# Kernel optimization log

Measured on AMD Instinct MI355X. Metric: run time of the kernel, lower is better.

The kernel has to match this reference:

```python
import jax, jax.numpy as jnp
import numpy as np

RANK = 64


def setup_inputs() -> dict:
    key = jax.random.key(0)
    ks = jax.random.split(key, 7)
    N, C, H, W, T = 32, 128, 32, 32, 12
    x = jax.random.normal(ks[0], (N, C, H, W, T), dtype=jnp.float32)
    ts_w = jax.random.normal(ks[1], (RANK, T, 3, 3), dtype=jnp.float32) * 0.1
    ts_b = jnp.zeros((RANK,), dtype=jnp.float32)
    tc_w = jax.random.normal(ks[2], (RANK, C), dtype=jnp.float32) * 0.1
    tc_b = jnp.zeros((RANK,), dtype=jnp.float32)
    sc_w = jax.random.normal(ks[3], (RANK, T), dtype=jnp.float32) * 0.1
    sc_b = jnp.zeros((RANK,), dtype=jnp.float32)
    return {"x": x, "ts_w": ts_w, "ts_b": ts_b, "tc_w": tc_w,
            "tc_b": tc_b, "sc_w": sc_w, "sc_b": sc_b}


def reference(x, ts_w, ts_b, tc_w, tc_b, sc_w, sc_b):
    # x: (N, C, H, W, T) -> internal layout (N, T, C, H, W)
    N, C, H, W, T = x.shape
    xt = jnp.transpose(x, (0, 4, 1, 2, 3))  # (N, T, C, H, W)

    # --- TS branch: channel-mean map -> conv(T -> rank, k3, pad1) -> sigmoid ---
    ts_in = jnp.mean(xt, axis=2)  # (N, T, H, W)
    ts = jax.lax.conv_general_dilated(
        ts_in, ts_w, window_strides=(1, 1), padding=[(1, 1), (1, 1)],
        dimension_numbers=("NCHW", "OIHW", "NCHW"))
    ts = ts + ts_b[None, :, None, None]
    TS = jax.nn.sigmoid(ts.reshape(N, RANK, H * W))  # (N, R, HW)

    # --- global spatial pooling: (N, T, C) ---
    pooled = jnp.mean(xt, axis=(3, 4))  # (N, T, C)

    # TC branch: Linear(C -> rank) then sigmoid -> (N, T, R)
    TC = jax.nn.sigmoid(pooled @ tc_w.T + tc_b)

    # SC branch: Linear(T -> rank) on (N, C, T) -> (N, C, R)
    SC = jax.nn.sigmoid(jnp.transpose(pooled, (0, 2, 1)) @ sc_w.T + sc_b)

    # rank-R CP reconstruction: result[n,t,c,s] = sum_r TS[n,r,s]*TC[n,t,r]*SC[n,c,r]
    result = jnp.einsum("nrs,ntr,ncr->ntcs", TS, TC, SC).reshape(N, T, C, H, W)

    res = jax.nn.relu(result * xt)  # (N, T, C, H, W)
    return jnp.transpose(res, (0, 2, 3, 4, 1))  # (N, C, H, W, T)
```

## Files before the change

kernel.cpp:

```cpp
#include <hip/hip_runtime.h>

#define N_ 32
#define C_ 128
#define H_ 32
#define W_ 32
#define T_ 12
#define R_ 64
#define HW_ (H_*W_)
#define HWT_ (HW_*T_)
#define CHWT_ ((size_t)C_*HW_*T_)
#define NCHUNK_ 16

__device__ __forceinline__ float sigm(float v) {
    return 1.0f / (1.0f + __expf(-v));
}

__global__ __launch_bounds__(256) void k_stats(const float* __restrict__ x,
                                               float* __restrict__ ts_in,
                                               float* __restrict__ pooled_p) {
    int chunk = blockIdx.x;
    int n = blockIdx.y;
    int tid = threadIdx.x;
    int wave = tid >> 6;
    int lane = tid & 63;
    int hw = chunk * 64 + lane;

    __shared__ float ts_l[4][64 * T_];

    const float* xb = x + (size_t)n * CHWT_ + (size_t)hw * T_;

    float ts_acc[T_];
    #pragma unroll
    for (int j = 0; j < T_; ++j) ts_acc[j] = 0.f;

    int g = lane & 15;
    int up1 = g & 1, up2 = g & 2, up4 = g & 4, up8 = g & 8;
    int trev = ((g & 1) << 3) | ((g & 2) << 1) | ((g & 4) >> 1) | ((g & 8) >> 3);
    bool do_store = (lane < 16) && (trev < T_);
    float* pp = pooled_p + ((size_t)(chunk * N_ + n) * T_ + trev) * C_;

    #pragma unroll 2
    for (int ci = 0; ci < 32; ++ci) {
        int c = wave + 4 * ci;
        const float4* p = (const float4*)(xb + (size_t)c * HWT_);
        float4 v0 = p[0], v1 = p[1], v2 = p[2];
        float v[T_] = {v0.x, v0.y, v0.z, v0.w,
                       v1.x, v1.y, v1.z, v1.w,
                       v2.x, v2.y, v2.z, v2.w};
        #pragma unroll
        for (int j = 0; j < T_; ++j) ts_acc[j] += v[j];

        float wv[16];
        #pragma unroll
        for (int j = 0; j < T_; ++j) {
            float s = v[j];
            s += __shfl_xor(s, 32, 64);
            s += __shfl_xor(s, 16, 64);
            wv[j] = s;
        }
        wv[12] = 0.f; wv[13] = 0.f; wv[14] = 0.f; wv[15] = 0.f;

        #pragma unroll
        for (int i = 0; i < 8; ++i) {
            float send = up1 ? wv[i] : wv[i + 8];
            float recv = __shfl_xor(send, 1, 64);
            wv[i] = (up1 ? wv[i + 8] : wv[i]) + recv;
        }
        #pragma unroll
        for (int i = 0; i < 4; ++i) {
            float send = up2 ? wv[i] : wv[i + 4];
            float recv = __shfl_xor(send, 2, 64);
            wv[i] = (up2 ? wv[i + 4] : wv[i]) + recv;
        }
        #pragma unroll
        for (int i = 0; i < 2; ++i) {
            float send = up4 ? wv[i] : wv[i + 2];
            float recv = __shfl_xor(send, 4, 64);
            wv[i] = (up4 ? wv[i + 2] : wv[i]) + recv;
        }
        {
            float send = up8 ? wv[0] : wv[1];
            float recv = __shfl_xor(send, 8, 64);
            wv[0] = (up8 ? wv[1] : wv[0]) + recv;
        }
        if (do_store) pp[c] = wv[0];
    }

    #pragma unroll
    for (int j = 0; j < T_; ++j) ts_l[wave][lane * T_ + j] = ts_acc[j];
    __syncthreads();

    for (int i = tid; i < 64 * T_; i += 256) {
        float s = ts_l[0][i] + ts_l[1][i] + ts_l[2][i] + ts_l[3][i];
        int hwl = i / T_;
        int t = i - hwl * T_;
        ts_in[(n * T_ + t) * HW_ + chunk * 64 + hwl] = s * (1.0f / 128.0f);
    }
}

__global__ __launch_bounds__(256) void k_mid(const float* __restrict__ ts_in,
                                             const float* __restrict__ ts_w,
                                             const float* __restrict__ ts_b,
                                             const float* __restrict__ pooled_p,
                                             const float* __restrict__ tc_w,
                                             const float* __restrict__ tc_b,
                                             const float* __restrict__ sc_w,
                                             const float* __restrict__ sc_b,
                                             float* __restrict__ TS,
                                             float* __restrict__ TC,
                                             float* __restrict__ SC) {
    int n = blockIdx.x;
    int part = blockIdx.y;
    int tid = threadIdx.x;
    __shared__ __align__(16) float smem[9728];

    if (part < 32) {
        int h = part;
        float* rows = smem;
        float* wl = smem + 1296;
        for (int i = tid; i < 3 * T_ * 36; i += 256) {
            int kh = i / (T_ * 36);
            int rem = i - kh * (T_ * 36);
            int t = rem / 36;
            int wp = rem - t * 36;
            int hr = h + kh - 1;
            float v = 0.f;
            if (wp >= 1 && wp <= 32 && hr >= 0 && hr < H_)
                v = ts_in[((n * T_ + t) * H_ + hr) * W_ + (wp - 1)];
            rows[i] = v;
        }
        for (int i = tid; i < R_ * 108; i += 256) wl[i] = ts_w[i];
        __syncthreads();
        int r = tid >> 2;
        int j = tid & 3;
        float acc[8];
        float b = ts_b[r];
        #pragma unroll
        for (int wi = 0; wi < 8; ++wi) acc[wi] = b;
        for (int t = 0; t < T_; ++t) {
            #pragma unroll
            for (int kh = 0; kh < 3; ++kh) {
                const float* rp = rows + (kh * T_ + t) * 36 + j * 8;
                float4 ra = *(const float4*)rp;
                float4 rb = *(const float4*)(rp + 4);
                float2 rc = *(const float2*)(rp + 8);
                float win[10] = {ra.x, ra.y, ra.z, ra.w,
                                 rb.x, rb.y, rb.z, rb.w, rc.x, rc.y};
                const float* wt = wl + r * 108 + t * 9 + kh * 3;
                float w0 = wt[0], w1 = wt[1], w2 = wt[2];
                #pragma unroll
                for (int wi = 0; wi < 8; ++wi)
                    acc[wi] += win[wi] * w0 + win[wi + 1] * w1 + win[wi + 2] * w2;
            }
        }
        float* outp = TS + (size_t)(n * R_ + r) * HW_ + h * W_ + j * 8;
        float4 o0 = {sigm(acc[0]), sigm(acc[1]), sigm(acc[2]), sigm(acc[3])};
        float4 o1 = {sigm(acc[4]), sigm(acc[5]), sigm(acc[6]), sigm(acc[7])};
        *(float4*)outp = o0;
        *(float4*)(outp + 4) = o1;
    } else if (part == 32) {
        float* pl = smem;
        float* twt = smem + 1536;
        for (int i = tid; i < T_ * C_; i += 256) {
            float s = 0.f;
            #pragma unroll
            for (int k = 0; k < NCHUNK_; ++k)
                s += pooled_p[((size_t)k * N_ + n) * (T_ * C_) + i];
            pl[i] = s * (1.0f / 1024.0f);
        }
        for (int i = tid; i < C_ * R_; i += 256) {
            int r = i >> 7;
            int c = i & 127;
            twt[c * R_ + r] = tc_w[i];
        }
        __syncthreads();
        for (int o = tid; o < T_ * R_; o += 256) {
            int t = o >> 6;
            int r = o & 63;
            float acc = tc_b[r];
            #pragma unroll 4
            for (int c = 0; c < C_; ++c) acc += pl[t * C_ + c] * twt[c * R_ + r];
            TC[n * T_ * R_ + o] = sigm(acc);
        }
    } else {
        int c0 = (part - 33) * 32;
        float* pl = smem;
        float* sw = smem + 1536;
        for (int i = tid; i < T_ * C_; i += 256) {
            float s = 0.f;
            #pragma unroll
            for (int k = 0; k < NCHUNK_; ++k)
                s += pooled_p[((size_t)k * N_ + n) * (T_ * C_) + i];
            pl[i] = s * (1.0f / 1024.0f);
        }
        for (int i = tid; i < R_ * T_; i += 256) sw[i] = sc_w[i];
        __syncthreads();
        for (int o = tid; o < 32 * R_; o += 256) {
            int c = c0 + (o >> 6);
            int r = o & 63;
            float acc = sc_b[r];
            #pragma unroll
            for (int t = 0; t < T_; ++t) acc += pl[t * C_ + c] * sw[r * T_ + t];
            SC[(size_t)n * C_ * R_ + c * R_ + r] = sigm(acc);
        }
    }
}

__global__ __launch_bounds__(192) void k_main(const float* __restrict__ x,
                                              const float* __restrict__ TS,
                                              const float* __restrict__ TC,
                                              const float* __restrict__ SC,
                                              float* __restrict__ out) {
    int schunk = blockIdx.x;
    int n = blockIdx.y;
    int chalf = blockIdx.z;
    int tid = threadIdx.x;
    __shared__ float tst[R_ * 16];
    __shared__ float tcl[T_ * R_];
    int s0 = schunk * 16;
    for (int i = tid; i < R_ * 16; i += 192) {
        int r = i >> 4;
        int sl = i & 15;
        tst[i] = TS[(size_t)(n * R_ + r) * HW_ + s0 + sl];
    }
    for (int i = tid; i < T_ * R_; i += 192) tcl[i] = TC[n * T_ * R_ + i];
    __syncthreads();
    int sl = tid / T_;
    int t = tid - sl * T_;
    float w[R_];
    #pragma unroll
    for (int r = 0; r < R_; ++r) w[r] = tcl[t * R_ + r] * tst[r * 16 + sl];
    size_t base = (size_t)n * CHWT_ + (size_t)s0 * T_ + tid;
    const float* scb = SC + (size_t)n * C_ * R_;

    int cbeg = chalf * 64;
    int cend = cbeg + 64;
    for (int cg = cbeg; cg < cend; cg += 4) {
        float xg[4];
        #pragma unroll
        for (int cc = 0; cc < 4; ++cc)
            xg[cc] = x[base + (size_t)(cg + cc) * HWT_];
        #pragma unroll
        for (int cc = 0; cc < 4; ++cc) {
            const float4* sp = (const float4*)(scb + (size_t)(cg + cc) * R_);
            float a0 = 0.f, a1 = 0.f, a2 = 0.f, a3 = 0.f;
            #pragma unroll
            for (int r4 = 0; r4 < R_ / 4; ++r4) {
                float4 q = sp[r4];
                a0 = fmaf(q.x, w[4 * r4 + 0], a0);
                a1 = fmaf(q.y, w[4 * r4 + 1], a1);
                a2 = fmaf(q.z, w[4 * r4 + 2], a2);
                a3 = fmaf(q.w, w[4 * r4 + 3], a3);
            }
            float acc = (a0 + a1) + (a2 + a3);
            float rr = acc * xg[cc];
            size_t idx = base + (size_t)(cg + cc) * HWT_;
            out[idx] = rr > 0.f ? rr : 0.f;
        }
    }
}

extern "C" void kernel_launch(void* const* d_in, const int* in_sizes, int n_in,
                              void* d_out, int out_size, void* d_ws, size_t ws_size,
                              hipStream_t stream) {
    const float* x    = (const float*)d_in[0];
    const float* ts_w = (const float*)d_in[1];
    const float* ts_b = (const float*)d_in[2];
    const float* tc_w = (const float*)d_in[3];
    const float* tc_b = (const float*)d_in[4];
    const float* sc_w = (const float*)d_in[5];
    const float* sc_b = (const float*)d_in[6];
    float* out = (float*)d_out;

    float* ws       = (float*)d_ws;
    float* ts_in    = ws;
    float* pooled_p = ts_in + 393216;
    float* TS       = pooled_p + 786432;
    float* TC       = TS + 2097152;
    float* SC       = TC + 24576;

    hipLaunchKernelGGL(k_stats, dim3(NCHUNK_, 32), dim3(256), 0, stream, x, ts_in, pooled_p);
    hipLaunchKernelGGL(k_mid, dim3(32, 37), dim3(256), 0, stream,
                       ts_in, ts_w, ts_b, pooled_p, tc_w, tc_b, sc_w, sc_b, TS, TC, SC);
    hipLaunchKernelGGL(k_main, dim3(64, 32, 2), dim3(192), 0, stream, x, TS, TC, SC, out);
}
```

Before: 537.5 us.

## Restructure main reconstruction as register-tiled shared-memory GEMM over rank

The main kernel now computes the rank-64 contraction as a small GEMM per (n, spatial chunk). SC is transposed into shared memory and the TS*TC outer-product weights are built there, in two 32-rank phases, and each thread accumulates an 8-channel by 12-(s,t) register tile. The old kernel had every thread reread SC rows with scalar FMA chains and kept 64 weights per thread. The new version reuses operands across a register tile and does float4 loads and stores of x and out. It uses more registers (96 accumulators) and more shared memory, which lowers occupancy, and the grid drops from 4096 to 2048 blocks.

```diff
diff --git a/kernel.cpp b/kernel.cpp
--- a/kernel.cpp
+++ b/kernel.cpp
@@ -206,57 +206,92 @@
     }
 }
 
-__global__ __launch_bounds__(192) void k_main(const float* __restrict__ x,
-                                              const float* __restrict__ TS,
-                                              const float* __restrict__ TC,
-                                              const float* __restrict__ SC,
-                                              float* __restrict__ out) {
+__global__ __launch_bounds__(256, 2) void k_main(const float* __restrict__ x,
+                                                 const float* __restrict__ TS,
+                                                 const float* __restrict__ TC,
+                                                 const float* __restrict__ SC,
+                                                 float* __restrict__ out) {
     int schunk = blockIdx.x;
     int n = blockIdx.y;
-    int chalf = blockIdx.z;
     int tid = threadIdx.x;
-    __shared__ float tst[R_ * 16];
-    __shared__ float tcl[T_ * R_];
     int s0 = schunk * 16;
-    for (int i = tid; i < R_ * 16; i += 192) {
-        int r = i >> 4;
-        int sl = i & 15;
-        tst[i] = TS[(size_t)(n * R_ + r) * HW_ + s0 + sl];
-    }
-    for (int i = tid; i < T_ * R_; i += 192) tcl[i] = TC[n * T_ * R_ + i];
-    __syncthreads();
-    int sl = tid / T_;
-    int t = tid - sl * T_;
-    float w[R_];
+
+    __shared__ __align__(16) float scT[32][128];
+    __shared__ __align__(16) float wls[32][192];
+    __shared__ float tss[R_ * 16];
+    __shared__ float tcs[T_ * R_];
+
+    for (int i = tid; i < R_ * 16; i += 256)
+        tss[i] = TS[(size_t)(n * R_ + (i >> 4)) * HW_ + s0 + (i & 15)];
+    for (int i = tid; i < T_ * R_; i += 256)
+        tcs[i] = TC[n * T_ * R_ + i];
+
+    const float* scb = SC + (size_t)n * C_ * R_;
+    int coct = tid >> 4;
+    int sloc = tid & 15;
+
+    float acc[8][12];
     #pragma unroll
-    for (int r = 0; r < R_; ++r) w[r] = tcl[t * R_ + r] * tst[r * 16 + sl];
-    size_t base = (size_t)n * CHWT_ + (size_t)s0 * T_ + tid;
-    const float* scb = SC + (size_t)n * C_ * R_;
-
-    int cbeg = chalf * 64;
-    int cend = cbeg + 64;
-    for (int cg = cbeg; cg < cend; cg += 4) {
-        float xg[4];
-        #pragma unroll
-        for (int cc = 0; cc < 4; ++cc)
-            xg[cc] = x[base + (size_t)(cg + cc) * HWT_];
-        #pragma unroll
-        for (int cc = 0; cc < 4; ++cc) {
-            const float4* sp = (const float4*)(scb + (size_t)(cg + cc) * R_);
-            float a0 = 0.f, a1 = 0.f, a2 = 0.f, a3 = 0.f;
-            #pragma unroll
-            for (int r4 = 0; r4 < R_ / 4; ++r4) {
-                float4 q = sp[r4];
-                a0 = fmaf(q.x, w[4 * r4 + 0], a0);
-                a1 = fmaf(q.y, w[4 * r4 + 1], a1);
-                a2 = fmaf(q.z, w[4 * r4 + 2], a2);
-                a3 = fmaf(q.w, w[4 * r4 + 3], a3);
-            }
-            float acc = (a0 + a1) + (a2 + a3);
-            float rr = acc * xg[cc];
-            size_t idx = base + (size_t)(cg + cc) * HWT_;
-            out[idx] = rr > 0.f ? rr : 0.f;
-        }
+    for (int ii = 0; ii < 8; ++ii)
+        #pragma unroll
+        for (int jj = 0; jj < 12; ++jj) acc[ii][jj] = 0.f;
+
+    for (int kk = 0; kk < 2; ++kk) {
+        int r0 = kk * 32;
+        __syncthreads();
+        for (int i = tid; i < 32 * 128; i += 256) {
+            int r = i >> 7, c = i & 127;
+            scT[r][c] = scb[c * R_ + r0 + r];
+        }
+        for (int i = tid; i < 32 * 192; i += 256) {
+            int r = i / 192;
+            int st = i - r * 192;
+            int s = st / 12;
+            int t = st - s * 12;
+            wls[r][st] = tss[(r0 + r) * 16 + s] * tcs[t * R_ + r0 + r];
+        }
+        __syncthreads();
+
+        #pragma unroll 2
+        for (int r = 0; r < 32; ++r) {
+            float4 a0 = *(const float4*)&scT[r][coct * 8];
+            float4 a1 = *(const float4*)&scT[r][coct * 8 + 4];
+            float4 b0 = *(const float4*)&wls[r][sloc * 12];
+            float4 b1 = *(const float4*)&wls[r][sloc * 12 + 4];
+            float4 b2 = *(const float4*)&wls[r][sloc * 12 + 8];
+            float av[8] = {a0.x, a0.y, a0.z, a0.w, a1.x, a1.y, a1.z, a1.w};
+            float bv[12] = {b0.x, b0.y, b0.z, b0.w,
+                            b1.x, b1.y, b1.z, b1.w,
+                            b2.x, b2.y, b2.z, b2.w};
+            #pragma unroll
+            for (int ii = 0; ii < 8; ++ii)
+                #pragma unroll
+                for (int jj = 0; jj < 12; ++jj)
+                    acc[ii][jj] = fmaf(av[ii], bv[jj], acc[ii][jj]);
+        }
+    }
+
+    size_t sbase = (size_t)n * CHWT_ + (size_t)(s0 + sloc) * T_;
+    #pragma unroll
+    for (int ii = 0; ii < 8; ++ii) {
+        int c = coct * 8 + ii;
+        const float4* xp = (const float4*)(x + sbase + (size_t)c * HWT_);
+        float4 x0 = xp[0], x1 = xp[1], x2 = xp[2];
+        float4 o0, o1, o2;
+        o0.x = acc[ii][0] * x0.x;  o0.y = acc[ii][1] * x0.y;
+        o0.z = acc[ii][2] * x0.z;  o0.w = acc[ii][3] * x0.w;
+        o1.x = acc[ii][4] * x1.x;  o1.y = acc[ii][5] * x1.y;
+        o1.z = acc[ii][6] * x1.z;  o1.w = acc[ii][7] * x1.w;
+        o2.x = acc[ii][8] * x2.x;  o2.y = acc[ii][9] * x2.y;
+        o2.z = acc[ii][10] * x2.z; o2.w = acc[ii][11] * x2.w;
+        o0.x = o0.x > 0.f ? o0.x : 0.f;  o0.y = o0.y > 0.f ? o0.y : 0.f;
+        o0.z = o0.z > 0.f ? o0.z : 0.f;  o0.w = o0.w > 0.f ? o0.w : 0.f;
+        o1.x = o1.x > 0.f ? o1.x : 0.f;  o1.y = o1.y > 0.f ? o1.y : 0.f;
+        o1.z = o1.z > 0.f ? o1.z : 0.f;  o1.w = o1.w > 0.f ? o1.w : 0.f;
+        o2.x = o2.x > 0.f ? o2.x : 0.f;  o2.y = o2.y > 0.f ? o2.y : 0.f;
+        o2.z = o2.z > 0.f ? o2.z : 0.f;  o2.w = o2.w > 0.f ? o2.w : 0.f;
+        float4* op = (float4*)(out + sbase + (size_t)c * HWT_);
+        op[0] = o0; op[1] = o1; op[2] = o2;
     }
 }
 
@@ -282,5 +317,5 @@
     hipLaunchKernelGGL(k_stats, dim3(NCHUNK_, 32), dim3(256), 0, stream, x, ts_in, pooled_p);
     hipLaunchKernelGGL(k_mid, dim3(32, 37), dim3(256), 0, stream,
                        ts_in, ts_w, ts_b, pooled_p, tc_w, tc_b, sc_w, sc_b, TS, TC, SC);
-    hipLaunchKernelGGL(k_main, dim3(64, 32, 2), dim3(192), 0, stream, x, TS, TC, SC, out);
-}
+    hipLaunchKernelGGL(k_main, dim3(64, 32), dim3(256), 0, stream, x, TS, TC, SC, out);
+}
```

New measurement: 469.9 us. 12.6% less time.
